# Performance work log

Measured on AMD Instinct MI355X. Metric: run time of the kernel, lower is better.

Reference implementation:

```python
import jax, jax.numpy as jnp
import numpy as np

B, S, D_MODEL, N_HEADS, D_K, D_V = 2, 2048, 1024, 16, 64, 64


def setup_inputs() -> dict:
    key = jax.random.key(0)
    k1, k2, k3, k4, k5, k6, k7 = jax.random.split(key, 7)
    scale = 1.0 / np.sqrt(D_MODEL)
    inputs = {
        "input_Q": jax.random.normal(k1, (B, S, D_MODEL), dtype=jnp.float32),
        "input_K": jax.random.normal(k2, (B, S, D_MODEL), dtype=jnp.float32),
        "input_V": jax.random.normal(k3, (B, S, D_MODEL), dtype=jnp.float32),
        # causal mask: True means position is masked out (matches masked_fill_)
        "attn_mask": jnp.broadcast_to(
            ~jnp.tril(jnp.ones((S, S), dtype=bool)), (B, S, S)
        ),
        "flag": 0,
        "W_Q": jax.random.normal(k4, (D_MODEL, N_HEADS * D_K), dtype=jnp.float32) * scale,
        "W_K": jax.random.normal(k5, (D_MODEL, N_HEADS * D_K), dtype=jnp.float32) * scale,
        "W_V": jax.random.normal(k6, (D_MODEL, N_HEADS * D_V), dtype=jnp.float32) * scale,
        "W_O": jax.random.normal(k7, (N_HEADS * D_V, D_MODEL), dtype=jnp.float32) * scale,
    }
    return inputs


def reference(input_Q, input_K, input_V, attn_mask, flag, W_Q, W_K, W_V, W_O):
    b = input_Q.shape[0]
    # project and split heads: [b, h, s, d]
    Q = (input_Q @ W_Q).reshape(b, -1, N_HEADS, D_K).transpose(0, 2, 1, 3)
    K = (input_K @ W_K).reshape(b, -1, N_HEADS, D_K).transpose(0, 2, 1, 3)
    V = (input_V @ W_V).reshape(b, -1, N_HEADS, D_V).transpose(0, 2, 1, 3)
    # scaled dot-product attention with additive large-negative masking
    scores = jnp.einsum("bhqd,bhkd->bhqk", Q, K) / np.sqrt(D_K).astype(np.float32)
    scores = jnp.where(attn_mask[:, None, :, :], jnp.float32(-1e9), scores)
    attn = jax.nn.softmax(scores, axis=-1)
    context = jnp.einsum("bhqk,bhkd->bhqd", attn, V)  # [b, h, s, d_v]
    context = context.transpose(0, 2, 1, 3).reshape(b, -1, N_HEADS * D_V)
    return context @ W_O
```

## Files before the change

### kernel.cpp

```cpp
#include <hip/hip_runtime.h>

#define DEVINL __device__ __forceinline__

typedef __attribute__((ext_vector_type(8))) short short8;
typedef __attribute__((ext_vector_type(4))) short sh4;
typedef __attribute__((ext_vector_type(4))) float floatx4;

constexpr int S_LEN = 2048;
constexpr int DM    = 1024;
constexpr int NHEAD = 16;
constexpr int DHEAD = 64;
constexpr int BATCH = 2;
constexpr int MROWS = BATCH * S_LEN;
constexpr float LOG2E = 1.44269504f;
constexpr float SM_C1 = 0.125f * LOG2E;
constexpr float SM_C2 = -24.0f * LOG2E;

#define MFMA16(a, b, c) __builtin_amdgcn_mfma_f32_16x16x16bf16_1k(a, b, c, 0, 0, 0)

DEVINL unsigned short f2bf(float x) {
  union { float f; unsigned u; } un; un.f = x;
  unsigned u = un.u;
  return (unsigned short)((u + 0x7fffu + ((u >> 16) & 1u)) >> 16);
}
DEVINL unsigned short f2bf_fast(float x) {
  union { float f; unsigned u; } un; un.f = x;
  return (unsigned short)((un.u + 0x8000u) >> 16);
}

__global__ __launch_bounds__(256) void prep_kernel(const float* __restrict__ s0,
                                                   const float* __restrict__ s1,
                                                   const float* __restrict__ s2,
                                                   unsigned short* __restrict__ d0,
                                                   unsigned short* __restrict__ d1,
                                                   unsigned short* __restrict__ d2,
                                                   const float* __restrict__ W0,
                                                   const float* __restrict__ W1,
                                                   const float* __restrict__ W2,
                                                   const float* __restrict__ W3,
                                                   unsigned short* __restrict__ T0,
                                                   unsigned short* __restrict__ T1,
                                                   unsigned short* __restrict__ T2,
                                                   unsigned short* __restrict__ T3) {
  __shared__ unsigned short tile[32][33];
  const int y = blockIdx.y;
  if (y < 3) {
    const float* s = y == 0 ? s0 : (y == 1 ? s1 : s2);
    unsigned short* d = y == 0 ? d0 : (y == 1 ? d1 : d2);
    int i = (blockIdx.x * 256 + threadIdx.x) * 4;
    float4 v = *(const float4*)(s + i);
    unsigned lo = (unsigned)f2bf(v.x) | ((unsigned)f2bf(v.y) << 16);
    unsigned hi = (unsigned)f2bf(v.z) | ((unsigned)f2bf(v.w) << 16);
    *(uint2*)(d + i) = make_uint2(lo, hi);
  } else {
    const int x = blockIdx.x;
    const int wsel = x >> 10, rem = x & 1023;
    const float* W = wsel == 0 ? W0 : (wsel == 1 ? W1 : (wsel == 2 ? W2 : W3));
    unsigned short* Wt = wsel == 0 ? T0 : (wsel == 1 ? T1 : (wsel == 2 ? T2 : T3));
    int t = threadIdx.x;
    int c = t & 31, r0 = t >> 5;
    int nB = (rem & 31) * 32, kB = (rem >> 5) * 32;
    for (int i = 0; i < 4; ++i) {
      int r = r0 + i * 8;
      tile[r][c] = f2bf(W[(size_t)(kB + r) * DM + nB + c]);
    }
    __syncthreads();
    for (int i = 0; i < 4; ++i) {
      int r = r0 + i * 8;
      Wt[(size_t)(nB + r) * DM + kB + c] = tile[c][r];
    }
  }
}

DEVINL void load_lds16(const unsigned short* g, unsigned short* l) {
  __builtin_amdgcn_global_load_lds((const __attribute__((address_space(1))) unsigned int*)g,
                                   (__attribute__((address_space(3))) unsigned int*)l,
                                   16, 0, 0);
}

template <int MODE>
DEVINL void gemm_body(const unsigned short* __restrict__ A,
                      const unsigned short* __restrict__ Bt,
                      void* __restrict__ Cout) {
  constexpr int K = 1024, N = 1024;
  __shared__ alignas(16) unsigned short As[128 * 32];
  __shared__ alignas(16) unsigned short Bs[128 * 32];
  const int tid  = threadIdx.x;
  const int wave = tid >> 6, lane = tid & 63;
  const int quad = lane >> 4, l16 = lane & 15;
  const int mBase = blockIdx.y * 128, nBase = blockIdx.x * 128;
  const int wm = (wave >> 1) * 64, wn = (wave & 1) * 64;
  const int sr = lane >> 2;
  const int sc = (lane & 3) * 8;
  floatx4 acc[4][4] = {};

  for (int k0 = 0; k0 < K; k0 += 32) {
    __syncthreads();
#pragma unroll
    for (int j = 0; j < 2; ++j) {
      int row = wave * 32 + j * 16 + sr;
      load_lds16(A  + (size_t)(mBase + row) * K + k0 + sc, As + (wave * 32 + j * 16) * 32);
      load_lds16(Bt + (size_t)(nBase + row) * K + k0 + sc, Bs + (wave * 32 + j * 16) * 32);
    }
    __syncthreads();
    short8 af[4], bfr[4];
#pragma unroll
    for (int mt = 0; mt < 4; ++mt) af[mt]  = *(const short8*)&As[(wm + mt * 16 + l16) * 32 + quad * 8];
#pragma unroll
    for (int nt = 0; nt < 4; ++nt) bfr[nt] = *(const short8*)&Bs[(wn + nt * 16 + l16) * 32 + quad * 8];
#pragma unroll
    for (int mt = 0; mt < 4; ++mt)
#pragma unroll
      for (int nt = 0; nt < 4; ++nt)
        acc[mt][nt] = __builtin_amdgcn_mfma_f32_16x16x32_bf16(af[mt], bfr[nt], acc[mt][nt], 0, 0, 0);
  }

#pragma unroll
  for (int mt = 0; mt < 4; ++mt)
#pragma unroll
    for (int nt = 0; nt < 4; ++nt) {
      const int m = mBase + wm + mt * 16 + quad * 4;
      const int n = nBase + wn + nt * 16 + l16;
      if (MODE == 2) {
        const int bq = m >> 11, s = m & 2047;
        const int hh = n >> 6,  d = n & 63;
        unsigned short w4[4];
#pragma unroll
        for (int r = 0; r < 4; ++r) w4[r] = f2bf(acc[mt][nt][r]);
        *(uint2*)&((unsigned short*)Cout)[((size_t)((bq * 16 + hh) * 64 + d)) * S_LEN + s] =
            *(const uint2*)w4;
      } else {
#pragma unroll
        for (int r = 0; r < 4; ++r) {
          if (MODE == 0) ((unsigned short*)Cout)[(size_t)(m + r) * N + n] = f2bf(acc[mt][nt][r]);
          else           ((float*)Cout)[(size_t)(m + r) * N + n]          = acc[mt][nt][r];
        }
      }
    }
}

__global__ __launch_bounds__(256) void gemm_qkv(const unsigned short* __restrict__ A0,
                                                const unsigned short* __restrict__ A1,
                                                const unsigned short* __restrict__ A2,
                                                const unsigned short* __restrict__ B0,
                                                const unsigned short* __restrict__ B1,
                                                const unsigned short* __restrict__ B2,
                                                unsigned short* __restrict__ C0,
                                                unsigned short* __restrict__ C1,
                                                unsigned short* __restrict__ C2) {
  const int z = blockIdx.z;
  if (z == 2)      gemm_body<2>(A2, B2, C2);
  else if (z == 1) gemm_body<0>(A1, B1, C1);
  else             gemm_body<0>(A0, B0, C0);
}

__global__ __launch_bounds__(256) void gemm_out64(const unsigned short* __restrict__ A,
                                                  const unsigned short* __restrict__ Bt,
                                                  float* __restrict__ C) {
  constexpr int K = 1024, N = 1024;
  __shared__ alignas(16) unsigned short As[64 * 32];
  __shared__ alignas(16) unsigned short Bs[128 * 32];
  const int tid  = threadIdx.x;
  const int wave = tid >> 6, lane = tid & 63;
  const int quad = lane >> 4, l16 = lane & 15;
  const int mBase = blockIdx.y * 64, nBase = blockIdx.x * 128;
  const int wm = (wave >> 1) * 32, wn = (wave & 1) * 64;
  const int sr = lane >> 2;
  const int sc = (lane & 3) * 8;
  floatx4 acc[2][4] = {};

  for (int k0 = 0; k0 < K; k0 += 32) {
    __syncthreads();
    load_lds16(A + (size_t)(mBase + wave * 16 + sr) * K + k0 + sc, As + (wave * 16) * 32);
#pragma unroll
    for (int j = 0; j < 2; ++j) {
      int row = wave * 32 + j * 16 + sr;
      load_lds16(Bt + (size_t)(nBase + row) * K + k0 + sc, Bs + (wave * 32 + j * 16) * 32);
    }
    __syncthreads();
    short8 af[2], bfr[4];
#pragma unroll
    for (int mt = 0; mt < 2; ++mt) af[mt]  = *(const short8*)&As[(wm + mt * 16 + l16) * 32 + quad * 8];
#pragma unroll
    for (int nt = 0; nt < 4; ++nt) bfr[nt] = *(const short8*)&Bs[(wn + nt * 16 + l16) * 32 + quad * 8];
#pragma unroll
    for (int mt = 0; mt < 2; ++mt)
#pragma unroll
      for (int nt = 0; nt < 4; ++nt)
        acc[mt][nt] = __builtin_amdgcn_mfma_f32_16x16x32_bf16(af[mt], bfr[nt], acc[mt][nt], 0, 0, 0);
  }

#pragma unroll
  for (int mt = 0; mt < 2; ++mt)
#pragma unroll
    for (int nt = 0; nt < 4; ++nt)
#pragma unroll
      for (int r = 0; r < 4; ++r) {
        int m = mBase + wm + mt * 16 + quad * 4 + r;
        int n = nBase + wn + nt * 16 + l16;
        C[(size_t)m * N + n] = acc[mt][nt][r];
      }
}

__global__ __launch_bounds__(256, 3) void attn_kernel(const unsigned short* __restrict__ Qp,
                                                      const unsigned short* __restrict__ Kp,
                                                      const unsigned short* __restrict__ Vtg,
                                                      unsigned short* __restrict__ ctx) {
  const int bh = blockIdx.y;
  const int b  = bh >> 4, h = bh & 15;
  const int tid = threadIdx.x;
  const int w = tid >> 6, lane = tid & 63;
  const int quad = lane >> 4, l16 = lane & 15;

  __shared__ float rsL[4][4][16];
  __shared__ alignas(16) float Ored[4][4][16][16];

  const unsigned short* Kbh = Kp  + (size_t)(b * S_LEN) * DM + h * DHEAD;
  const unsigned short* Vbh = Vtg + (size_t)(bh * DHEAD) * S_LEN;

  const unsigned short* kf = Kbh + (size_t)(w * 16 + l16) * DM + quad * 8;
  const unsigned short* vf = Vbh + (size_t)l16 * S_LEN + w * 16 + quad * 4;

  short8 kc0 = *(const short8*)kf;
  short8 kc1 = *(const short8*)(kf + 32);
  sh4 vv[4];
#pragma unroll
  for (int dt = 0; dt < 4; ++dt)
    vv[dt] = *(const sh4*)(vf + (size_t)(dt * 16) * S_LEN);

#pragma unroll 1
  for (int half = 0; half < 2; ++half) {
    const int qt = half ? (int)blockIdx.x : 31 - (int)blockIdx.x;
    const int Q0 = qt * 64;
    const int nT = qt + 1;

    short8 qB[4][2];
#pragma unroll
    for (int nt = 0; nt < 4; ++nt) {
      const size_t qr = ((size_t)(b * S_LEN + Q0 + nt * 16 + l16)) * DM + h * DHEAD + quad * 8;
      qB[nt][0] = *(const short8*)&Qp[qr];
      qB[nt][1] = *(const short8*)&Qp[qr + 32];
    }

    floatx4 o[4][4] = {};
    float rs[4] = {0.f, 0.f, 0.f, 0.f};

#pragma unroll 1
    for (int t = 0; t < nT; ++t) {
      const int tn = (t + 1 < nT) ? t + 1 : 0;
      const size_t ko = (size_t)tn * 64 * DM;
      short8 nk0 = *(const short8*)(kf + ko);
      short8 nk1 = *(const short8*)(kf + ko + 32);
      sh4 nv[4];
#pragma unroll
      for (int dt = 0; dt < 4; ++dt)
        nv[dt] = *(const sh4*)(vf + (size_t)(dt * 16) * S_LEN + tn * 64);

      const bool masked = (t == nT - 1);
      const int sbase = w * 16 + quad * 4;

#pragma unroll
      for (int nt = 0; nt < 4; ++nt) {
        floatx4 sc = {};
        sc = __builtin_amdgcn_mfma_f32_16x16x32_bf16(kc0, qB[nt][0], sc, 0, 0, 0);
        sc = __builtin_amdgcn_mfma_f32_16x16x32_bf16(kc1, qB[nt][1], sc, 0, 0, 0);
        const int qoff = nt * 16 + l16;
        sh4 pa;
        float acc = 0.f;
#pragma unroll
        for (int r = 0; r < 4; ++r) {
          float p = __builtin_amdgcn_exp2f(fmaf(sc[r], SM_C1, SM_C2));
          if (masked && (sbase + r > qoff)) p = 0.f;
          acc += p;
          pa[r] = (short)f2bf_fast(p);
        }
        rs[nt] += acc;
#pragma unroll
        for (int dt = 0; dt < 4; ++dt)
          o[nt][dt] = MFMA16(pa, vv[dt], o[nt][dt]);
      }

      kc0 = nk0;
      kc1 = nk1;
#pragma unroll
      for (int dt = 0; dt < 4; ++dt) vv[dt] = nv[dt];
    }

#pragma unroll
    for (int nt = 0; nt < 4; ++nt) {
      rs[nt] += __shfl_xor(rs[nt], 16, 64);
      rs[nt] += __shfl_xor(rs[nt], 32, 64);
    }
    if (quad == 0) {
#pragma unroll
      for (int nt = 0; nt < 4; ++nt) rsL[w][nt][l16] = rs[nt];
    }

    for (int nt = 0; nt < 4; ++nt) {
      __syncthreads();
#pragma unroll
      for (int dt = 0; dt < 4; ++dt)
        *(floatx4*)&Ored[w][dt][l16][quad * 4] = o[nt][dt];
      __syncthreads();
      floatx4 acc = {};
#pragma unroll
      for (int w2 = 0; w2 < 4; ++w2) {
        floatx4 v = *(const floatx4*)&Ored[w2][w][l16][quad * 4];
#pragma unroll
        for (int j = 0; j < 4; ++j) acc[j] += v[j];
      }
#pragma unroll
      for (int j = 0; j < 4; ++j) {
        const int q16 = quad * 4 + j;
        float l = rsL[0][nt][q16] + rsL[1][nt][q16] + rsL[2][nt][q16] + rsL[3][nt][q16];
        const size_t row = (size_t)(b * S_LEN + Q0 + nt * 16 + q16);
        ctx[row * DM + h * DHEAD + w * 16 + l16] = f2bf(acc[j] / l);
      }
    }
  }
}

extern "C" void kernel_launch(void* const* d_in, const int* in_sizes, int n_in,
                              void* d_out, int out_size, void* d_ws, size_t ws_size,
                              hipStream_t stream) {
  const float* Xq = (const float*)d_in[0];
  const float* Xk = (const float*)d_in[1];
  const float* Xv = (const float*)d_in[2];
  const float* Wq = (const float*)d_in[5];
  const float* Wk = (const float*)d_in[6];
  const float* Wv = (const float*)d_in[7];
  const float* Wo = (const float*)d_in[8];
  float* out = (float*)d_out;

  char* ws = (char*)d_ws;
  constexpr size_t XBYTES = (size_t)MROWS * DM * 2;
  constexpr size_t WBYTES = (size_t)DM * DM * 2;
  unsigned short* xq_bf = (unsigned short*)(ws);
  unsigned short* xk_bf = (unsigned short*)(ws + XBYTES);
  unsigned short* xv_bf = (unsigned short*)(ws + 2 * XBYTES);
  unsigned short* wqt   = (unsigned short*)(ws + 3 * XBYTES);
  unsigned short* wkt   = (unsigned short*)(ws + 3 * XBYTES + WBYTES);
  unsigned short* wvt   = (unsigned short*)(ws + 3 * XBYTES + 2 * WBYTES);
  unsigned short* wot   = (unsigned short*)(ws + 3 * XBYTES + 3 * WBYTES);
  unsigned short* qp    = (unsigned short*)(ws + 3 * XBYTES + 4 * WBYTES);
  unsigned short* kp    = (unsigned short*)(ws + 4 * XBYTES + 4 * WBYTES);
  unsigned short* vt    = (unsigned short*)(ws + 5 * XBYTES + 4 * WBYTES);
  unsigned short* ctx   = xq_bf;

  prep_kernel<<<dim3(4096, 4), 256, 0, stream>>>(Xq, Xk, Xv, xq_bf, xk_bf, xv_bf,
                                                 Wq, Wk, Wv, Wo, wqt, wkt, wvt, wot);

  gemm_qkv<<<dim3(DM / 128, MROWS / 128, 3), 256, 0, stream>>>(
      xq_bf, xk_bf, xv_bf, wqt, wkt, wvt, qp, kp, vt);

  attn_kernel<<<dim3(16, BATCH * NHEAD), 256, 0, stream>>>(qp, kp, vt, ctx);

  gemm_out64<<<dim3(DM / 128, MROWS / 64), 256, 0, stream>>>(ctx, wot, out);
}
```

Baseline: 247.2 us.

## Stage K/V tiles through double-buffered swizzled LDS with direct global-to-LDS loads

The attention kernel no longer has each wave load its own K and V fragments into registers for prefetch. Two waves stage K and two stage V into a double-buffered shared-memory tile using direct global-to-LDS loads, with an XOR swizzle to avoid bank conflicts. A barrier is added per key tile, and the Ored reduction buffer is padded to reduce bank conflicts. This trades register pressure and scattered per-wave global loads for coalesced cooperative loads, at the cost of a barrier every iteration and extra LDS use that may lower occupancy.

```diff
diff --git a/kernel.cpp b/kernel.cpp
--- a/kernel.cpp
+++ b/kernel.cpp
@@ -131,10 +131,8 @@
             *(const uint2*)w4;
       } else {
 #pragma unroll
-        for (int r = 0; r < 4; ++r) {
-          if (MODE == 0) ((unsigned short*)Cout)[(size_t)(m + r) * N + n] = f2bf(acc[mt][nt][r]);
-          else           ((float*)Cout)[(size_t)(m + r) * N + n]          = acc[mt][nt][r];
-        }
+        for (int r = 0; r < 4; ++r)
+          ((unsigned short*)Cout)[(size_t)(m + r) * N + n] = f2bf(acc[mt][nt][r]);
       }
     }
 }
@@ -212,21 +210,45 @@
   const int w = tid >> 6, lane = tid & 63;
   const int quad = lane >> 4, l16 = lane & 15;
 
+  __shared__ alignas(16) unsigned short KVs[2 * 8192];
   __shared__ float rsL[4][4][16];
-  __shared__ alignas(16) float Ored[4][4][16][16];
+  __shared__ alignas(16) float Ored[4][4][16][20];
 
   const unsigned short* Kbh = Kp  + (size_t)(b * S_LEN) * DM + h * DHEAD;
   const unsigned short* Vbh = Vtg + (size_t)(bh * DHEAD) * S_LEN;
 
-  const unsigned short* kf = Kbh + (size_t)(w * 16 + l16) * DM + quad * 8;
-  const unsigned short* vf = Vbh + (size_t)l16 * S_LEN + w * 16 + quad * 4;
-
-  short8 kc0 = *(const short8*)kf;
-  short8 kc1 = *(const short8*)(kf + 32);
-  sh4 vv[4];
-#pragma unroll
-  for (int dt = 0; dt < 4; ++dt)
-    vv[dt] = *(const sh4*)(vf + (size_t)(dt * 16) * S_LEN);
+  int srow[4], scol[4];
+#pragma unroll
+  for (int j = 0; j < 4; ++j) {
+    const int p = (w & 1) * 256 + j * 64 + lane;
+    srow[j] = p >> 3;
+    scol[j] = ((p & 7) ^ (srow[j] & 7)) * 8;
+  }
+  const bool stageK = (w < 2);
+
+  const int swz = l16 & 7;
+  const int kRow = (w * 16 + l16) * 64;
+  const int kOff0 = kRow + ((0 + quad) ^ swz) * 8;
+  const int kOff1 = kRow + ((4 + quad) ^ swz) * 8;
+  int vOff[4];
+#pragma unroll
+  for (int dt = 0; dt < 4; ++dt) {
+    const int ch = 2 * w + (quad >> 1);
+    vOff[dt] = 4096 + (dt * 16 + l16) * 64 + (ch ^ swz) * 8 + (quad & 1) * 4;
+  }
+
+  {
+    unsigned short* dst = KVs + w * 2048;
+#pragma unroll
+    for (int j = 0; j < 4; ++j) {
+      const unsigned short* src = stageK
+          ? Kbh + (size_t)srow[j] * DM + scol[j]
+          : Vbh + (size_t)srow[j] * S_LEN + scol[j];
+      load_lds16(src, dst + j * 512);
+    }
+  }
+
+  int cur = 0;
 
 #pragma unroll 1
   for (int half = 0; half < 2; ++half) {
@@ -247,14 +269,27 @@
 
 #pragma unroll 1
     for (int t = 0; t < nT; ++t) {
-      const int tn = (t + 1 < nT) ? t + 1 : 0;
-      const size_t ko = (size_t)tn * 64 * DM;
-      short8 nk0 = *(const short8*)(kf + ko);
-      short8 nk1 = *(const short8*)(kf + ko + 32);
-      sh4 nv[4];
-#pragma unroll
-      for (int dt = 0; dt < 4; ++dt)
-        nv[dt] = *(const sh4*)(vf + (size_t)(dt * 16) * S_LEN + tn * 64);
+      __syncthreads();
+
+      {
+        const int tn = (t + 1 < nT) ? t + 1 : 0;
+        const int kb = tn * 64;
+        unsigned short* dst = KVs + (cur ^ 1) * 8192 + w * 2048;
+#pragma unroll
+        for (int j = 0; j < 4; ++j) {
+          const unsigned short* src = stageK
+              ? Kbh + (size_t)(kb + srow[j]) * DM + scol[j]
+              : Vbh + (size_t)srow[j] * S_LEN + kb + scol[j];
+          load_lds16(src, dst + j * 512);
+        }
+      }
+
+      const unsigned short* buf = KVs + cur * 8192;
+      short8 kc0 = *(const short8*)&buf[kOff0];
+      short8 kc1 = *(const short8*)&buf[kOff1];
+      sh4 vv[4];
+#pragma unroll
+      for (int dt = 0; dt < 4; ++dt) vv[dt] = *(const sh4*)&buf[vOff[dt]];
 
       const bool masked = (t == nT - 1);
       const int sbase = w * 16 + quad * 4;
@@ -280,10 +315,7 @@
           o[nt][dt] = MFMA16(pa, vv[dt], o[nt][dt]);
       }
 
-      kc0 = nk0;
-      kc1 = nk1;
-#pragma unroll
-      for (int dt = 0; dt < 4; ++dt) vv[dt] = nv[dt];
+      cur ^= 1;
     }
 
 #pragma unroll
```

New measurement: 239.0 us. 1.03x faster.
